# Performance work log

Measured on AMD Instinct MI355X. Metric: run time of the kernel, lower is better.

## Reference

```python
import jax, jax.numpy as jnp
import numpy as np

KH = KW = 3
STRIDE = 2
PAD = 1


def _extract_patches(x, kh, kw, stride, pad):
    # x: [B, C, H, W] -> patches [B, C, Ho, Wo, kh*kw]
    B, C, H, W = x.shape
    xp = jnp.pad(x, ((0, 0), (0, 0), (pad, pad), (pad, pad)))
    Ho = (H + 2 * pad - kh) // stride + 1
    Wo = (W + 2 * pad - kw) // stride + 1
    cols = [
        xp[:, :, i : i + stride * Ho : stride, j : j + stride * Wo : stride]
        for i in range(kh)
        for j in range(kw)
    ]
    return jnp.stack(cols, axis=-1)  # [B, C, Ho, Wo, kh*kw]


def setup_inputs() -> dict:
    key = jax.random.key(0)
    k1, k2 = jax.random.split(key)
    x = jax.random.normal(k1, (32, 64, 112, 112), dtype=jnp.float32)
    s = jax.random.normal(k2, (64, KH, KW), dtype=jnp.float32) * 0.1
    return {"x": x, "s": s}


def reference(x, s):
    # RRSVM rank-weighted pooling: for each sliding window, sort values
    # descending and take a weighted sum with per-channel rank weights s.
    patches = _extract_patches(x, KH, KW, STRIDE, PAD)  # [B,C,Ho,Wo,K]
    order = jnp.argsort(-patches, axis=-1)              # descending ranks
    sorted_vals = jnp.take_along_axis(patches, order, axis=-1)
    s_flat = s.reshape(s.shape[0], KH * KW)             # [C, K]
    out = jnp.einsum("bchwk,ck->bchw", sorted_vals, s_flat)
    return out, order.astype(jnp.int64)
```

## Files before the change

kernel.cpp:

```cpp
#include <hip/hip_runtime.h>


typedef float nfloat4 __attribute__((ext_vector_type(4)));

constexpr int B  = 32;
constexpr int C  = 64;
constexpr int H  = 112;
constexpr int W  = 112;
constexpr int HO = 56;
constexpr int WO = 56;
constexpr int KK = 9;
constexpr int NPIX = HO * WO;
constexpr int BLK  = 256;
constexpr int LROW = 128;
constexpr int RPT  = 4;
constexpr int IR   = 2 * RPT + 1;

__global__ __launch_bounds__(BLK) void rrsvm_kernel(
    const float* __restrict__ x, const float* __restrict__ s,
    float* __restrict__ out, float* __restrict__ order)
{
    __shared__ float lx[IR * LROW];
    __shared__ float lorder[RPT * WO * KK];

    const int plane = blockIdx.y;
    const int ho0   = blockIdx.x;
    const int tid   = threadIdx.x;
    const int w     = tid >> 6;
    const int lane  = tid & 63;
    const int c     = plane & (C - 1);

    const float* xp = x + (size_t)plane * (H * W);

    if (tid < IR * (W / 4)) {
        const int r  = tid / (W / 4);
        const int cc = tid - r * (W / 4);
        const int grow = 8 * ho0 - 1 + r;
        nfloat4 val = (nfloat4)0.0f;
        if ((unsigned)grow < (unsigned)H)
            val = *(const nfloat4*)(xp + grow * W + 4 * cc);
        float* dst = &lx[r * LROW + 1 + 4 * cc];
        dst[0] = val.x; dst[1] = val.y; dst[2] = val.z; dst[3] = val.w;
    }
    if (tid < IR) lx[tid * LROW] = 0.0f;
    __syncthreads();

    const bool live = (lane < WO);
    const int  lc   = live ? lane : 0;
    const int  ho   = ho0 * RPT + w;

    float v[KK];
    float fid[KK];
#pragma unroll
    for (int dy = 0; dy < 3; ++dy)
#pragma unroll
        for (int dx = 0; dx < 3; ++dx) {
            const int k = dy * 3 + dx;
            v[k]   = lx[(2 * w + dy) * LROW + 2 * lc + dx];
            fid[k] = (float)k;
        }

    auto CE = [&](int a, int b) {
        const float va = v[a],   vb = v[b];
        const float fa = fid[a], fb = fid[b];
        const bool sw = (va < vb) || ((va == vb) && (fa > fb));
        v[a]   = fmaxf(va, vb);
        v[b]   = fminf(va, vb);
        fid[a] = sw ? fb : fa;
        fid[b] = sw ? fa : fb;
    };
    CE(0,1); CE(2,3); CE(4,5); CE(6,7);
    CE(0,2); CE(1,3); CE(4,6); CE(5,7);
    CE(1,2); CE(5,6);
    CE(0,4); CE(1,5); CE(2,6); CE(3,7);
    CE(2,4); CE(3,5);
    CE(1,2); CE(3,4); CE(5,6);
    CE(7,8); CE(6,7); CE(5,6); CE(4,5); CE(3,4); CE(2,3); CE(1,2); CE(0,1);

    const float* sc = s + c * KK;
    float acc = 0.0f;
#pragma unroll
    for (int k = 0; k < KK; ++k) acc = fmaf(v[k], sc[k], acc);

    if (live) {
        const int widx = w * WO + lane;
#pragma unroll
        for (int k = 0; k < KK; ++k)
            lorder[widx * KK + k] = fid[k];
    }
    __syncthreads();

    nfloat4* __restrict__ ob =
        (nfloat4*)(order + ((size_t)plane * NPIX + (size_t)ho0 * RPT * WO) * KK);
    const nfloat4* __restrict__ lb = (const nfloat4*)lorder;
#pragma unroll
    for (int i = tid; i < RPT * WO * KK / 4; i += BLK)
        __builtin_nontemporal_store(lb[i], ob + i);

    if (live)
        __builtin_nontemporal_store(acc, out + (size_t)plane * NPIX + ho * WO + lane);
}

extern "C" void kernel_launch(void* const* d_in, const int* in_sizes, int n_in,
                              void* d_out, int out_size, void* d_ws, size_t ws_size,
                              hipStream_t stream) {
    const float* x = (const float*)d_in[0];
    const float* s = (const float*)d_in[1];
    float* out   = (float*)d_out;
    float* order = out + (size_t)B * C * NPIX;

    dim3 grid(HO / RPT, B * C);
    rrsvm_kernel<<<grid, dim3(BLK), 0, stream>>>(x, s, out, order);
}
```

Measured before the change: 313.3 us.

## Load input windows directly from global and make order staging wave-local

Removes the shared-memory staging of input rows, so each thread reads its nine window values straight from global memory with clamped addressing and zero padding. The order write-out is now done per wavefront, each wave copying only its own output row, so both block-wide barriers become a single LDS waitcnt. Launch bounds now request 8 blocks per SM. The cost is more, less coalesced global loads that rely on the cache for reuse, and correctness now depends on each wave reading only the LDS it wrote itself.

```diff
diff --git a/kernel.cpp b/kernel.cpp
--- a/kernel.cpp
+++ b/kernel.cpp
@@ -12,15 +12,12 @@
 constexpr int KK = 9;
 constexpr int NPIX = HO * WO;
 constexpr int BLK  = 256;
-constexpr int LROW = 128;
 constexpr int RPT  = 4;
-constexpr int IR   = 2 * RPT + 1;
 
-__global__ __launch_bounds__(BLK) void rrsvm_kernel(
+__global__ __launch_bounds__(BLK, 8) void rrsvm_kernel(
     const float* __restrict__ x, const float* __restrict__ s,
     float* __restrict__ out, float* __restrict__ order)
 {
-    __shared__ float lx[IR * LROW];
     __shared__ float lorder[RPT * WO * KK];
 
     const int plane = blockIdx.y;
@@ -30,35 +27,29 @@
     const int lane  = tid & 63;
     const int c     = plane & (C - 1);
 
-    const float* xp = x + (size_t)plane * (H * W);
-
-    if (tid < IR * (W / 4)) {
-        const int r  = tid / (W / 4);
-        const int cc = tid - r * (W / 4);
-        const int grow = 8 * ho0 - 1 + r;
-        nfloat4 val = (nfloat4)0.0f;
-        if ((unsigned)grow < (unsigned)H)
-            val = *(const nfloat4*)(xp + grow * W + 4 * cc);
-        float* dst = &lx[r * LROW + 1 + 4 * cc];
-        dst[0] = val.x; dst[1] = val.y; dst[2] = val.z; dst[3] = val.w;
-    }
-    if (tid < IR) lx[tid * LROW] = 0.0f;
-    __syncthreads();
-
     const bool live = (lane < WO);
     const int  lc   = live ? lane : 0;
     const int  ho   = ho0 * RPT + w;
 
+    const float* xp = x + (size_t)plane * (H * W);
+
     float v[KK];
     float fid[KK];
 #pragma unroll
-    for (int dy = 0; dy < 3; ++dy)
+    for (int dy = 0; dy < 3; ++dy) {
+        const int r  = 2 * ho - 1 + dy;
+        const int rr = r < 0 ? 0 : r;
+        const float* rp = xp + rr * W;
 #pragma unroll
         for (int dx = 0; dx < 3; ++dx) {
-            const int k = dy * 3 + dx;
-            v[k]   = lx[(2 * w + dy) * LROW + 2 * lc + dx];
+            const int k  = dy * 3 + dx;
+            const int cl = 2 * lc - 1 + dx;
+            const int cc = cl < 0 ? 0 : cl;
+            const float val = rp[cc];
+            v[k]   = (r >= 0 && cl >= 0) ? val : 0.0f;
             fid[k] = (float)k;
         }
+    }
 
     auto CE = [&](int a, int b) {
         const float va = v[a],   vb = v[b];
@@ -88,13 +79,14 @@
         for (int k = 0; k < KK; ++k)
             lorder[widx * KK + k] = fid[k];
     }
-    __syncthreads();
 
+    asm volatile("s_waitcnt lgkmcnt(0)" ::: "memory");
+
+    const nfloat4* __restrict__ lb = (const nfloat4*)&lorder[w * WO * KK];
     nfloat4* __restrict__ ob =
-        (nfloat4*)(order + ((size_t)plane * NPIX + (size_t)ho0 * RPT * WO) * KK);
-    const nfloat4* __restrict__ lb = (const nfloat4*)lorder;
+        (nfloat4*)(order + ((size_t)plane * NPIX + (size_t)ho * WO) * KK);
 #pragma unroll
-    for (int i = tid; i < RPT * WO * KK / 4; i += BLK)
+    for (int i = lane; i < WO * KK / 4; i += 64)
         __builtin_nontemporal_store(lb[i], ob + i);
 
     if (live)
```

Measured after the change: 320.3 us. 1.02x slower.
